# Optimization experiments

Hardware: AMD Instinct MI355X
Metric: run time of the kernel (lower is better)

Reference implementation:

```python
import jax, jax.numpy as jnp
import numpy as np

NUM_HEADS = 8
HEAD_DIM = 64
EMBED = NUM_HEADS * HEAD_DIM  # 512


def setup_inputs() -> dict:
    key = jax.random.key(0)
    ks = jax.random.split(key, 8)
    B, S = 4, 2048
    s = 1.0 / np.sqrt(HEAD_DIM)
    so = 1.0 / np.sqrt(EMBED)
    return {
        "queries": jax.random.normal(ks[0], (B, S, EMBED), jnp.float32),
        "keys": jax.random.normal(ks[1], (B, S, EMBED), jnp.float32),
        "values": jax.random.normal(ks[2], (B, S, EMBED), jnp.float32),
        "Wq": jax.random.uniform(ks[3], (HEAD_DIM, HEAD_DIM), jnp.float32, -s, s),
        "Wk": jax.random.uniform(ks[4], (HEAD_DIM, HEAD_DIM), jnp.float32, -s, s),
        "Wv": jax.random.uniform(ks[5], (HEAD_DIM, HEAD_DIM), jnp.float32, -s, s),
        "Wo": jax.random.uniform(ks[6], (EMBED, EMBED), jnp.float32, -so, so),
        "bo": jax.random.uniform(ks[7], (EMBED,), jnp.float32, -so, so),
    }


def reference(queries, keys, values, Wq, Wk, Wv, Wo, bo):
    B, Sq, _ = queries.shape
    # Faithful to source: keys/values are (buggily) reshaped from `queries`;
    # with equal seq lens this means k/v come from the queries tensor.
    q = queries.reshape(B, Sq, NUM_HEADS, HEAD_DIM)
    k = q
    v = q
    # per-head linear: torch Linear(x) = x @ W.T
    q = jnp.einsum('bshd,ed->bshe', q, Wq)
    k = jnp.einsum('bshd,ed->bshe', k, Wk)
    v = jnp.einsum('bshd,ed->bshe', v, Wv)
    sim = jnp.einsum('bqhd,bkhd->bhqk', q, k)  # [B,H,Sq,Sk]
    attn = jax.nn.softmax(sim * (1.0 / np.sqrt(HEAD_DIM)), axis=-1)
    out = jnp.einsum('bhqk,bkhd->bqhd', attn, v)
    out = out.reshape(B, Sq, EMBED)
    return out @ Wo.T + bo
```

## Files before the change

kernel.cpp:

```cpp
#include <hip/hip_runtime.h>
#include <cstddef>

#define S_ 2048
#define E_ 512

typedef __attribute__((ext_vector_type(8)))  short bf16x8;
typedef __attribute__((ext_vector_type(16))) float f32x16;

__device__ __forceinline__ unsigned short f2bf(float f) {
    union { float f; unsigned u; } v; v.f = f;
    return (unsigned short)((v.u + 0x7FFFu + ((v.u >> 16) & 1u)) >> 16);
}
__device__ __forceinline__ unsigned pk2bf(float a, float b) {
    union { float f; unsigned u; } x, y; x.f = a; y.f = b;
    return __builtin_amdgcn_perm(y.u + 0x8000u, x.u + 0x8000u, 0x07060302u);
}

__global__ __launch_bounds__(256) void prep_w(const float* __restrict__ Wq,
                                              const float* __restrict__ Wk,
                                              const float* __restrict__ Wo,
                                              const float* __restrict__ Wv,
                                              unsigned short* __restrict__ GT,
                                              unsigned short* __restrict__ W2) {
    int bi = blockIdx.x;
    if (bi < 16) {
        int idx = bi * 256 + threadIdx.x;
        int c = idx >> 6, d = idx & 63;
        float acc = 0.f;
#pragma unroll 8
        for (int e = 0; e < 64; ++e) acc += Wq[e * 64 + d] * Wk[e * 64 + c];
        GT[c * 64 + d] = f2bf(acc * 0.18033688011112042f);
    } else {
        int idx = (bi - 16) * 256 + threadIdx.x;
        int e = idx >> 9, f = idx & 511;
        int h = f >> 6, c = f & 63;
        const float* wo = Wo + e * 512 + h * 64;
        float acc = 0.f;
#pragma unroll 8
        for (int d = 0; d < 64; ++d) acc += wo[d] * Wv[d * 64 + c];
        W2[idx] = f2bf(acc);
    }
}

__global__ __launch_bounds__(256) void prep_X(const float* __restrict__ X,
                                              unsigned short* __restrict__ Xbf,
                                              unsigned short* __restrict__ XTg) {
    __shared__ unsigned short T[64][72];
    const int tid = threadIdx.x;
    const int st = blockIdx.x & 31, h = (blockIdx.x >> 5) & 7, b = blockIdx.x >> 8;
    const int s0 = st * 64;
    const int j = tid >> 2, g = tid & 3;
    const float* src = X + ((size_t)(b * S_ + s0 + j) * E_) + h * 64 + g * 16;
    unsigned short us[16];
#pragma unroll
    for (int i = 0; i < 16; i += 4) {
        float4 f = *(const float4*)(src + i);
        us[i] = f2bf(f.x); us[i + 1] = f2bf(f.y);
        us[i + 2] = f2bf(f.z); us[i + 3] = f2bf(f.w);
    }
    size_t xb = ((size_t)(b * S_ + s0 + j) * E_) + h * 64 + g * 16;
    *(uint4*)&Xbf[xb]     = *(uint4*)&us[0];
    *(uint4*)&Xbf[xb + 8] = *(uint4*)&us[8];
#pragma unroll
    for (int i = 0; i < 16; ++i) T[g * 16 + i][j] = us[i];
    __syncthreads();
    const int d = tid >> 2;
    size_t tb = ((size_t)((b * 8 + h) * 64 + d)) * S_ + s0 + g * 16;
    *(uint4*)&XTg[tb]     = *(uint4*)&T[d][g * 16];
    *(uint4*)&XTg[tb + 8] = *(uint4*)&T[d][g * 16 + 8];
}

__global__ __launch_bounds__(256, 2) void attn_mfma(const unsigned short* __restrict__ Xbf,
                                                    const unsigned short* __restrict__ XTg,
                                                    const unsigned short* __restrict__ GT,
                                                    unsigned short* __restrict__ AObf) {
    __shared__ unsigned short Ubf[128][72];
    __shared__ unsigned short Xrm[64][72];
    __shared__ unsigned short XT [64][72];
    __shared__ unsigned short Pbf[128][72];

    const int tid = threadIdx.x;
    const int w = tid >> 6, lane = tid & 63;
    const int lm = lane & 31, lh = lane >> 5;
    const int qt = blockIdx.x & 15, h = (blockIdx.x >> 4) & 7, b = blockIdx.x >> 7;
    const int s0 = qt * 128;

    {
        const int r = tid >> 1, c = (tid & 1) * 32;
        const unsigned short* src = Xbf + ((size_t)(b * S_ + s0 + r)) * E_ + h * 64 + c;
        unsigned short* dst = (r < 64) ? &Xrm[r][c] : &XT[r - 64][c];
#pragma unroll
        for (int u = 0; u < 4; ++u) *(uint4*)(dst + u * 8) = *(const uint4*)(src + u * 8);
    }
    __syncthreads();

    {
        f32x16 uacc[2];
#pragma unroll
        for (int nt = 0; nt < 2; ++nt)
#pragma unroll
            for (int i = 0; i < 16; ++i) uacc[nt][i] = 0.f;
        const int q = 32 * w + lm;
        const unsigned short* arow = (q < 64) ? &Xrm[q][0] : &XT[q - 64][0];
#pragma unroll
        for (int ks = 0; ks < 4; ++ks) {
            bf16x8 aX = *(const bf16x8*)(arow + ks * 16 + lh * 8);
#pragma unroll
            for (int nt = 0; nt < 2; ++nt) {
                bf16x8 bG = *(const bf16x8*)&GT[(lm + 32 * nt) * 64 + ks * 16 + lh * 8];
                uacc[nt] = __builtin_amdgcn_mfma_f32_32x32x16_bf16(aX, bG, uacc[nt], 0, 0, 0);
            }
        }
#pragma unroll
        for (int nt = 0; nt < 2; ++nt)
#pragma unroll
            for (int r = 0; r < 16; ++r) {
                int qrow = (r & 3) + 8 * (r >> 2) + 4 * lh;
                Ubf[32 * w + qrow][lm + 32 * nt] = f2bf(uacc[nt][r]);
            }
    }

    float lsum = 0.f;
    f32x16 AO[2];
#pragma unroll
    for (int nt = 0; nt < 2; ++nt)
#pragma unroll
        for (int i = 0; i < 16; ++i) AO[nt][i] = 0.f;

    for (int sk = 0; sk < S_; sk += 64) {
        __syncthreads();
        {
            const int r = tid >> 2, c = (tid & 3) * 16;
            const unsigned short* src = Xbf + ((size_t)(b * S_ + sk + r)) * E_ + h * 64 + c;
            *(uint4*)&Xrm[r][c]     = *(const uint4*)src;
            *(uint4*)&Xrm[r][c + 8] = *(const uint4*)(src + 8);
            const unsigned short* srct = XTg + ((size_t)((b * 8 + h) * 64 + r)) * S_ + sk + c;
            *(uint4*)&XT[r][c]      = *(const uint4*)srct;
            *(uint4*)&XT[r][c + 8]  = *(const uint4*)(srct + 8);
        }
        __syncthreads();

        f32x16 sc[2];
#pragma unroll
        for (int mt = 0; mt < 2; ++mt)
#pragma unroll
            for (int i = 0; i < 16; ++i) sc[mt][i] = 0.f;
#pragma unroll
        for (int ks = 0; ks < 4; ++ks) {
            bf16x8 bU = *(const bf16x8*)&Ubf[32 * w + lm][ks * 16 + lh * 8];
#pragma unroll
            for (int mt = 0; mt < 2; ++mt) {
                bf16x8 aX = *(const bf16x8*)&Xrm[32 * mt + lm][ks * 16 + lh * 8];
                sc[mt] = __builtin_amdgcn_mfma_f32_32x32x16_bf16(aX, bU, sc[mt], 0, 0, 0);
            }
        }

#pragma unroll
        for (int mt = 0; mt < 2; ++mt)
#pragma unroll
            for (int rg = 0; rg < 4; ++rg) {
                float p0 = exp2f(sc[mt][rg * 4 + 0]);
                float p1 = exp2f(sc[mt][rg * 4 + 1]);
                float p2 = exp2f(sc[mt][rg * 4 + 2]);
                float p3 = exp2f(sc[mt][rg * 4 + 3]);
                lsum += (p0 + p1) + (p2 + p3);
                unsigned u01 = pk2bf(p0, p1), u23 = pk2bf(p2, p3);
                int kc = 32 * mt + 8 * rg + 4 * lh;
                *(uint2*)&Pbf[32 * w + lm][kc] = make_uint2(u01, u23);
            }

#pragma unroll
        for (int js = 0; js < 4; ++js) {
            bf16x8 aP = *(const bf16x8*)&Pbf[32 * w + lm][js * 16 + lh * 8];
#pragma unroll
            for (int nt = 0; nt < 2; ++nt) {
                bf16x8 bX = *(const bf16x8*)&XT[lm + 32 * nt][js * 16 + lh * 8];
                AO[nt] = __builtin_amdgcn_mfma_f32_32x32x16_bf16(aP, bX, AO[nt], 0, 0, 0);
            }
        }
    }

    lsum += __shfl_xor(lsum, 32);
    float linv = 1.0f / lsum;
    float lrow[16];
#pragma unroll
    for (int r = 0; r < 16; ++r)
        lrow[r] = __shfl(linv, (r & 3) + 8 * (r >> 2) + 4 * lh);
#pragma unroll
    for (int nt = 0; nt < 2; ++nt)
#pragma unroll
        for (int r = 0; r < 16; ++r) {
            int qrow = (r & 3) + 8 * (r >> 2) + 4 * lh;
            Pbf[32 * w + qrow][lm + 32 * nt] = f2bf(AO[nt][r] * lrow[r]);
        }
    __syncthreads();
    {
        const int r = tid >> 1, c = (tid & 1) * 32;
        unsigned short* dst = AObf + ((size_t)(b * S_ + s0 + r)) * E_ + h * 64 + c;
#pragma unroll
        for (int u = 0; u < 4; ++u)
            *(uint4*)(dst + u * 8) = *(const uint4*)&Pbf[r][c + u * 8];
    }
}

__global__ __launch_bounds__(256) void out_gemm_bf(const unsigned short* __restrict__ A,
                                                   const unsigned short* __restrict__ W2,
                                                   const float* __restrict__ bo,
                                                   float* __restrict__ out) {
    __shared__ unsigned short At[64][72];
    __shared__ unsigned short Bt[64][72];
    typedef __attribute__((ext_vector_type(4))) float f32x4;
    const int tid = threadIdx.x;
    const int w = tid >> 6, lane = tid & 63;
    const int quad = lane >> 4, qidx = lane & 15;
    const int et = blockIdx.x & 7, rt = blockIdx.x >> 3;
    const int r0 = rt * 64, e0 = et * 64;
    const int jj = tid >> 2, g = tid & 3;
    f32x4 acc[4] = {{0,0,0,0},{0,0,0,0},{0,0,0,0},{0,0,0,0}};

    for (int k0 = 0; k0 < 512; k0 += 64) {
        __syncthreads();
        {
            const unsigned short* sa = A + (size_t)(r0 + jj) * 512 + k0 + g * 16;
            *(uint4*)&At[jj][g * 16]     = *(const uint4*)sa;
            *(uint4*)&At[jj][g * 16 + 8] = *(const uint4*)(sa + 8);
            const unsigned short* sb = W2 + (size_t)(e0 + jj) * 512 + k0 + g * 16;
            *(uint4*)&Bt[jj][g * 16]     = *(const uint4*)sb;
            *(uint4*)&Bt[jj][g * 16 + 8] = *(const uint4*)(sb + 8);
        }
        __syncthreads();
#pragma unroll
        for (int ks = 0; ks < 2; ++ks) {
            bf16x8 aA = *(const bf16x8*)&At[16 * w + qidx][ks * 32 + quad * 8];
#pragma unroll
            for (int nt = 0; nt < 4; ++nt) {
                bf16x8 bW = *(const bf16x8*)&Bt[qidx + 16 * nt][ks * 32 + quad * 8];
                acc[nt] = __builtin_amdgcn_mfma_f32_16x16x32_bf16(aA, bW, acc[nt], 0, 0, 0);
            }
        }
    }
#pragma unroll
    for (int nt = 0; nt < 4; ++nt) {
        float bv = bo[e0 + qidx + 16 * nt];
#pragma unroll
        for (int r = 0; r < 4; ++r)
            out[(size_t)(r0 + 16 * w + quad * 4 + r) * 512 + e0 + qidx + 16 * nt] =
                acc[nt][r] + bv;
    }
}

extern "C" void kernel_launch(void* const* d_in, const int* in_sizes, int n_in,
                              void* d_out, int out_size, void* d_ws, size_t ws_size,
                              hipStream_t stream) {
    (void)in_sizes; (void)n_in; (void)out_size; (void)ws_size;
    const float* X  = (const float*)d_in[0];
    const float* Wq = (const float*)d_in[3];
    const float* Wk = (const float*)d_in[4];
    const float* Wv = (const float*)d_in[5];
    const float* Wo = (const float*)d_in[6];
    const float* bo = (const float*)d_in[7];

    float* ws = (float*)d_ws;
    unsigned short* W2bf = (unsigned short*)ws;
    unsigned short* GT   = (unsigned short*)(ws + 131072);
    unsigned short* Xbf  = (unsigned short*)(ws + 133120);
    unsigned short* XTg  = (unsigned short*)(ws + 133120 + 2097152);
    unsigned short* AObf = (unsigned short*)(ws + 133120 + 4194304);

    prep_w   <<<1040, 256, 0, stream>>>(Wq, Wk, Wo, Wv, GT, W2bf);
    prep_X   <<<1024, 256, 0, stream>>>(X, Xbf, XTg);
    attn_mfma<<<512,  256, 0, stream>>>(Xbf, XTg, GT, AObf);
    out_gemm_bf<<<1024, 256, 0, stream>>>(AObf, W2bf, bo, (float*)d_out);
}
```

Baseline: 188.0 us.

## Keep P and U in registers, union LDS buffers, retile output GEMM

The attention kernel now keeps the softmax probabilities and the projected-query fragments in registers instead of round-tripping them through LDS. To line the register layout up with the MFMA operand layout it swaps the operand roles (X^T as A, P as B) and permutes the columns of XT during prep. LDS buffers are unioned and the launch bound is raised to 4 blocks per CU for higher occupancy. The output GEMM switches to 32x32 MFMA tiles of 64x128 with half the blocks. The permutation trick adds layout coupling between kernels, and the occupancy hint may force register spills.

Result: faster. 181.1 us (-3.7%).

```diff
diff --git a/kernel.cpp b/kernel.cpp
--- a/kernel.cpp
+++ b/kernel.cpp
@@ -65,19 +65,24 @@
     for (int i = 0; i < 16; ++i) T[g * 16 + i][j] = us[i];
     __syncthreads();
     const int d = tid >> 2;
+    const int pm[16] = {0,1,2,3,8,9,10,11,4,5,6,7,12,13,14,15};
+    unsigned short o[16];
+#pragma unroll
+    for (int i = 0; i < 16; ++i) o[i] = T[d][g * 16 + pm[i]];
     size_t tb = ((size_t)((b * 8 + h) * 64 + d)) * S_ + s0 + g * 16;
-    *(uint4*)&XTg[tb]     = *(uint4*)&T[d][g * 16];
-    *(uint4*)&XTg[tb + 8] = *(uint4*)&T[d][g * 16 + 8];
-}
-
-__global__ __launch_bounds__(256, 2) void attn_mfma(const unsigned short* __restrict__ Xbf,
+    *(uint4*)&XTg[tb]     = *(uint4*)&o[0];
+    *(uint4*)&XTg[tb + 8] = *(uint4*)&o[8];
+}
+
+__global__ __launch_bounds__(256, 4) void attn_mfma(const unsigned short* __restrict__ Xbf,
                                                     const unsigned short* __restrict__ XTg,
                                                     const unsigned short* __restrict__ GT,
                                                     unsigned short* __restrict__ AObf) {
-    __shared__ unsigned short Ubf[128][72];
-    __shared__ unsigned short Xrm[64][72];
-    __shared__ unsigned short XT [64][72];
-    __shared__ unsigned short Pbf[128][72];
+    __shared__ union SM {
+        unsigned short Q[128][72];
+        struct { unsigned short Xrm[64][72], XT[64][72]; } c;
+        unsigned short AOt[128][72];
+    } sm;
 
     const int tid = threadIdx.x;
     const int w = tid >> 6, lane = tid & 63;
@@ -88,55 +93,57 @@
     {
         const int r = tid >> 1, c = (tid & 1) * 32;
         const unsigned short* src = Xbf + ((size_t)(b * S_ + s0 + r)) * E_ + h * 64 + c;
-        unsigned short* dst = (r < 64) ? &Xrm[r][c] : &XT[r - 64][c];
-#pragma unroll
-        for (int u = 0; u < 4; ++u) *(uint4*)(dst + u * 8) = *(const uint4*)(src + u * 8);
-    }
-    __syncthreads();
-
+#pragma unroll
+        for (int u = 0; u < 4; ++u) *(uint4*)&sm.Q[r][c + u * 8] = *(const uint4*)(src + u * 8);
+    }
+    __syncthreads();
+
+    bf16x8 Ufrag[4];
     {
-        f32x16 uacc[2];
+        f32x16 ua[2];
 #pragma unroll
         for (int nt = 0; nt < 2; ++nt)
 #pragma unroll
-            for (int i = 0; i < 16; ++i) uacc[nt][i] = 0.f;
-        const int q = 32 * w + lm;
-        const unsigned short* arow = (q < 64) ? &Xrm[q][0] : &XT[q - 64][0];
+            for (int i = 0; i < 16; ++i) ua[nt][i] = 0.f;
 #pragma unroll
         for (int ks = 0; ks < 4; ++ks) {
-            bf16x8 aX = *(const bf16x8*)(arow + ks * 16 + lh * 8);
+            bf16x8 aQ = *(const bf16x8*)&sm.Q[32 * w + lm][ks * 16 + lh * 8];
 #pragma unroll
             for (int nt = 0; nt < 2; ++nt) {
                 bf16x8 bG = *(const bf16x8*)&GT[(lm + 32 * nt) * 64 + ks * 16 + lh * 8];
-                uacc[nt] = __builtin_amdgcn_mfma_f32_32x32x16_bf16(aX, bG, uacc[nt], 0, 0, 0);
+                ua[nt] = __builtin_amdgcn_mfma_f32_32x32x16_bf16(aQ, bG, ua[nt], 0, 0, 0);
             }
         }
 #pragma unroll
         for (int nt = 0; nt < 2; ++nt)
 #pragma unroll
-            for (int r = 0; r < 16; ++r) {
-                int qrow = (r & 3) + 8 * (r >> 2) + 4 * lh;
-                Ubf[32 * w + qrow][lm + 32 * nt] = f2bf(uacc[nt][r]);
-            }
+            for (int r = 0; r < 16; ++r)
+                sm.Q[32 * w + (r & 3) + 8 * (r >> 2) + 4 * lh][lm + 32 * nt] = f2bf(ua[nt][r]);
+#pragma unroll
+        for (int ks = 0; ks < 4; ++ks)
+            Ufrag[ks] = *(const bf16x8*)&sm.Q[32 * w + lm][ks * 16 + lh * 8];
     }
 
     float lsum = 0.f;
     f32x16 AO[2];
 #pragma unroll
-    for (int nt = 0; nt < 2; ++nt)
-#pragma unroll
-        for (int i = 0; i < 16; ++i) AO[nt][i] = 0.f;
+    for (int mt = 0; mt < 2; ++mt)
+#pragma unroll
+        for (int i = 0; i < 16; ++i) AO[mt][i] = 0.f;
+
+    const unsigned short* srcX = Xbf + ((size_t)(b * S_ + (tid >> 2))) * E_ + h * 64 + (tid & 3) * 16;
+    const unsigned short* srcT = XTg + ((size_t)((b * 8 + h) * 64 + (tid >> 2))) * S_ + (tid & 3) * 16;
 
     for (int sk = 0; sk < S_; sk += 64) {
         __syncthreads();
         {
+            const unsigned short* sx = srcX + (size_t)sk * E_;
             const int r = tid >> 2, c = (tid & 3) * 16;
-            const unsigned short* src = Xbf + ((size_t)(b * S_ + sk + r)) * E_ + h * 64 + c;
-            *(uint4*)&Xrm[r][c]     = *(const uint4*)src;
-            *(uint4*)&Xrm[r][c + 8] = *(const uint4*)(src + 8);
-            const unsigned short* srct = XTg + ((size_t)((b * 8 + h) * 64 + r)) * S_ + sk + c;
-            *(uint4*)&XT[r][c]      = *(const uint4*)srct;
-            *(uint4*)&XT[r][c + 8]  = *(const uint4*)(srct + 8);
+            *(uint4*)&sm.c.Xrm[r][c]     = *(const uint4*)sx;
+            *(uint4*)&sm.c.Xrm[r][c + 8] = *(const uint4*)(sx + 8);
+            const unsigned short* st = srcT + sk;
+            *(uint4*)&sm.c.XT[r][c]      = *(const uint4*)st;
+            *(uint4*)&sm.c.XT[r][c + 8]  = *(const uint4*)(st + 8);
         }
         __syncthreads();
 
@@ -146,52 +153,52 @@
 #pragma unroll
             for (int i = 0; i < 16; ++i) sc[mt][i] = 0.f;
 #pragma unroll
-        for (int ks = 0; ks < 4; ++ks) {
-            bf16x8 bU = *(const bf16x8*)&Ubf[32 * w + lm][ks * 16 + lh * 8];
+        for (int ks = 0; ks < 4; ++ks)
 #pragma unroll
             for (int mt = 0; mt < 2; ++mt) {
-                bf16x8 aX = *(const bf16x8*)&Xrm[32 * mt + lm][ks * 16 + lh * 8];
-                sc[mt] = __builtin_amdgcn_mfma_f32_32x32x16_bf16(aX, bU, sc[mt], 0, 0, 0);
-            }
-        }
-
+                bf16x8 aX = *(const bf16x8*)&sm.c.Xrm[32 * mt + lm][ks * 16 + lh * 8];
+                sc[mt] = __builtin_amdgcn_mfma_f32_32x32x16_bf16(aX, Ufrag[ks], sc[mt], 0, 0, 0);
+            }
+
+        unsigned up[16];
 #pragma unroll
         for (int mt = 0; mt < 2; ++mt)
 #pragma unroll
-            for (int rg = 0; rg < 4; ++rg) {
-                float p0 = exp2f(sc[mt][rg * 4 + 0]);
-                float p1 = exp2f(sc[mt][rg * 4 + 1]);
-                float p2 = exp2f(sc[mt][rg * 4 + 2]);
-                float p3 = exp2f(sc[mt][rg * 4 + 3]);
+            for (int qq = 0; qq < 4; ++qq) {
+                float p0 = exp2f(sc[mt][qq * 4 + 0]);
+                float p1 = exp2f(sc[mt][qq * 4 + 1]);
+                float p2 = exp2f(sc[mt][qq * 4 + 2]);
+                float p3 = exp2f(sc[mt][qq * 4 + 3]);
                 lsum += (p0 + p1) + (p2 + p3);
-                unsigned u01 = pk2bf(p0, p1), u23 = pk2bf(p2, p3);
-                int kc = 32 * mt + 8 * rg + 4 * lh;
-                *(uint2*)&Pbf[32 * w + lm][kc] = make_uint2(u01, u23);
+                up[mt * 8 + 2 * qq]     = pk2bf(p0, p1);
+                up[mt * 8 + 2 * qq + 1] = pk2bf(p2, p3);
             }
 
 #pragma unroll
         for (int js = 0; js < 4; ++js) {
-            bf16x8 aP = *(const bf16x8*)&Pbf[32 * w + lm][js * 16 + lh * 8];
-#pragma unroll
-            for (int nt = 0; nt < 2; ++nt) {
-                bf16x8 bX = *(const bf16x8*)&XT[lm + 32 * nt][js * 16 + lh * 8];
-                AO[nt] = __builtin_amdgcn_mfma_f32_32x32x16_bf16(aP, bX, AO[nt], 0, 0, 0);
+            union { unsigned u[4]; bf16x8 v; } bP;
+            bP.u[0] = up[js * 4 + 0]; bP.u[1] = up[js * 4 + 1];
+            bP.u[2] = up[js * 4 + 2]; bP.u[3] = up[js * 4 + 3];
+#pragma unroll
+            for (int mt = 0; mt < 2; ++mt) {
+                bf16x8 aT = *(const bf16x8*)&sm.c.XT[32 * mt + lm][js * 16 + lh * 8];
+                AO[mt] = __builtin_amdgcn_mfma_f32_32x32x16_bf16(aT, bP.v, AO[mt], 0, 0, 0);
             }
         }
     }
 
     lsum += __shfl_xor(lsum, 32);
     float linv = 1.0f / lsum;
-    float lrow[16];
-#pragma unroll
-    for (int r = 0; r < 16; ++r)
-        lrow[r] = __shfl(linv, (r & 3) + 8 * (r >> 2) + 4 * lh);
-#pragma unroll
-    for (int nt = 0; nt < 2; ++nt)
-#pragma unroll
-        for (int r = 0; r < 16; ++r) {
-            int qrow = (r & 3) + 8 * (r >> 2) + 4 * lh;
-            Pbf[32 * w + qrow][lm + 32 * nt] = f2bf(AO[nt][r] * lrow[r]);
+    __syncthreads();
+#pragma unroll
+    for (int mt = 0; mt < 2; ++mt)
+#pragma unroll
+        for (int qq = 0; qq < 4; ++qq) {
+            int d0 = 32 * mt + 8 * qq + 4 * lh;
+            *(unsigned*)&sm.AOt[32 * w + lm][d0] =
+                pk2bf(AO[mt][qq * 4 + 0] * linv, AO[mt][qq * 4 + 1] * linv);
+            *(unsigned*)&sm.AOt[32 * w + lm][d0 + 2] =
+                pk2bf(AO[mt][qq * 4 + 2] * linv, AO[mt][qq * 4 + 3] * linv);
         }
     __syncthreads();
     {
@@ -199,7 +206,7 @@
         unsigned short* dst = AObf + ((size_t)(b * S_ + s0 + r)) * E_ + h * 64 + c;
 #pragma unroll
         for (int u = 0; u < 4; ++u)
-            *(uint4*)(dst + u * 8) = *(const uint4*)&Pbf[r][c + u * 8];
+            *(uint4*)(dst + u * 8) = *(const uint4*)&sm.AOt[r][c + u * 8];
     }
 }
 
@@ -208,45 +215,50 @@
                                                    const float* __restrict__ bo,
                                                    float* __restrict__ out) {
     __shared__ unsigned short At[64][72];
-    __shared__ unsigned short Bt[64][72];
-    typedef __attribute__((ext_vector_type(4))) float f32x4;
+    __shared__ unsigned short Bt[128][72];
     const int tid = threadIdx.x;
     const int w = tid >> 6, lane = tid & 63;
-    const int quad = lane >> 4, qidx = lane & 15;
-    const int et = blockIdx.x & 7, rt = blockIdx.x >> 3;
-    const int r0 = rt * 64, e0 = et * 64;
-    const int jj = tid >> 2, g = tid & 3;
-    f32x4 acc[4] = {{0,0,0,0},{0,0,0,0},{0,0,0,0},{0,0,0,0}};
+    const int lm = lane & 31, lh = lane >> 5;
+    const int et = blockIdx.x & 3, rt = blockIdx.x >> 2;
+    const int r0 = rt * 64, e0 = et * 128;
+    f32x16 acc[2];
+#pragma unroll
+    for (int mt = 0; mt < 2; ++mt)
+#pragma unroll
+        for (int i = 0; i < 16; ++i) acc[mt][i] = 0.f;
 
     for (int k0 = 0; k0 < 512; k0 += 64) {
         __syncthreads();
         {
-            const unsigned short* sa = A + (size_t)(r0 + jj) * 512 + k0 + g * 16;
-            *(uint4*)&At[jj][g * 16]     = *(const uint4*)sa;
-            *(uint4*)&At[jj][g * 16 + 8] = *(const uint4*)(sa + 8);
-            const unsigned short* sb = W2 + (size_t)(e0 + jj) * 512 + k0 + g * 16;
-            *(uint4*)&Bt[jj][g * 16]     = *(const uint4*)sb;
-            *(uint4*)&Bt[jj][g * 16 + 8] = *(const uint4*)(sb + 8);
-        }
-        __syncthreads();
-#pragma unroll
-        for (int ks = 0; ks < 2; ++ks) {
-            bf16x8 aA = *(const bf16x8*)&At[16 * w + qidx][ks * 32 + quad * 8];
-#pragma unroll
-            for (int nt = 0; nt < 4; ++nt) {
-                bf16x8 bW = *(const bf16x8*)&Bt[qidx + 16 * nt][ks * 32 + quad * 8];
-                acc[nt] = __builtin_amdgcn_mfma_f32_16x16x32_bf16(aA, bW, acc[nt], 0, 0, 0);
-            }
-        }
-    }
-#pragma unroll
-    for (int nt = 0; nt < 4; ++nt) {
-        float bv = bo[e0 + qidx + 16 * nt];
-#pragma unroll
-        for (int r = 0; r < 4; ++r)
-            out[(size_t)(r0 + 16 * w + quad * 4 + r) * 512 + e0 + qidx + 16 * nt] =
-                acc[nt][r] + bv;
-    }
+            const int r = tid >> 2, c = (tid & 3) * 16;
+            const unsigned short* sa = A + (size_t)(r0 + r) * 512 + k0 + c;
+            *(uint4*)&At[r][c]     = *(const uint4*)sa;
+            *(uint4*)&At[r][c + 8] = *(const uint4*)(sa + 8);
+            const int r2 = tid >> 1, c2 = (tid & 1) * 32;
+            const unsigned short* sb = W2 + (size_t)(e0 + r2) * 512 + k0 + c2;
+#pragma unroll
+            for (int u = 0; u < 4; ++u)
+                *(uint4*)&Bt[r2][c2 + u * 8] = *(const uint4*)(sb + u * 8);
+        }
+        __syncthreads();
+#pragma unroll
+        for (int ks = 0; ks < 4; ++ks) {
+            bf16x8 bW = *(const bf16x8*)&Bt[32 * w + lm][ks * 16 + lh * 8];
+#pragma unroll
+            for (int mt = 0; mt < 2; ++mt) {
+                bf16x8 aA = *(const bf16x8*)&At[32 * mt + lm][ks * 16 + lh * 8];
+                acc[mt] = __builtin_amdgcn_mfma_f32_32x32x16_bf16(aA, bW, acc[mt], 0, 0, 0);
+            }
+        }
+    }
+    float bv = bo[e0 + 32 * w + lm];
+#pragma unroll
+    for (int mt = 0; mt < 2; ++mt)
+#pragma unroll
+        for (int r = 0; r < 16; ++r) {
+            int srow = r0 + 32 * mt + (r & 3) + 8 * (r >> 2) + 4 * lh;
+            out[(size_t)srow * 512 + e0 + 32 * w + lm] = acc[mt][r] + bv;
+        }
 }
 
 extern "C" void kernel_launch(void* const* d_in, const int* in_sizes, int n_in,
@@ -267,8 +279,8 @@
     unsigned short* XTg  = (unsigned short*)(ws + 133120 + 2097152);
     unsigned short* AObf = (unsigned short*)(ws + 133120 + 4194304);
 
-    prep_w   <<<1040, 256, 0, stream>>>(Wq, Wk, Wo, Wv, GT, W2bf);
-    prep_X   <<<1024, 256, 0, stream>>>(X, Xbf, XTg);
-    attn_mfma<<<512,  256, 0, stream>>>(Xbf, XTg, GT, AObf);
-    out_gemm_bf<<<1024, 256, 0, stream>>>(AObf, W2bf, bo, (float*)d_out);
-}
+    prep_w     <<<1040, 256, 0, stream>>>(Wq, Wk, Wo, Wv, GT, W2bf);
+    prep_X     <<<1024, 256, 0, stream>>>(X, Xbf, XTg);
+    attn_mfma  <<<512,  256, 0, stream>>>(Xbf, XTg, GT, AObf);
+    out_gemm_bf<<<512,  256, 0, stream>>>(AObf, W2bf, bo, (float*)d_out);
+}
```
